# Performance work log

Hardware: AMD Instinct MI355X
Metric: run time of the kernel (lower is better)

## Reference

```python
import jax, jax.numpy as jnp
import numpy as np

B, H, S, D = 2, 16, 8192, 128
NUM_REFLECTIONS = D // 2
ROPE_BASE = 10000.0


def setup_inputs() -> dict:
    key = jax.random.key(0)
    kq, kk, kv = jax.random.split(key, 3)
    q = jax.random.normal(kq, (B, H, S, D), dtype=jnp.float32)
    k = jax.random.normal(kk, (B, H, S, D), dtype=jnp.float32)
    vs = jax.random.normal(kv, (NUM_REFLECTIONS, D), dtype=jnp.float32) * 0.02
    # standard RoPE cos/sin buffer, rotate-half layout: angles duplicated over both halves
    inv_freq = 1.0 / (ROPE_BASE ** (jnp.arange(0, D, 2, dtype=jnp.float32) / D))  # [D/2]
    ang = jnp.arange(S, dtype=jnp.float32)[:, None] * inv_freq[None, :]           # [S, D/2]
    emb = jnp.concatenate([ang, ang], axis=-1)                                    # [S, D]
    cos = jnp.broadcast_to(jnp.cos(emb)[None], (B, S, D))
    sin = jnp.broadcast_to(jnp.sin(emb)[None], (B, S, D))
    return {"q": q, "k": k, "vs": vs, "cos": cos, "sin": sin}


def _householder_matrix(vs):
    # Q = prod of Householder reflections applied left-to-right, as in get_matrix()
    eye = jnp.eye(vs.shape[-1], dtype=vs.dtype)
    def step(Q, v):
        v_norm_sq = jnp.sum(v * v) + 1e-8
        Q = Q - (2.0 / v_norm_sq) * jnp.outer(v, v @ Q)
        return Q, None
    Q, _ = jax.lax.scan(step, eye, vs)
    return Q


def _rotate_half(x):
    d2 = x.shape[-1] // 2
    return jnp.concatenate([-x[..., d2:], x[..., :d2]], axis=-1)


def reference(q, k, vs, cos, sin):
    Q = _householder_matrix(vs)                 # [D, D]
    # inverse transform: x @ Q.T
    qi = jnp.einsum("bhsd,ed->bhse", q, Q)
    ki = jnp.einsum("bhsd,ed->bhse", k, Q)
    c = cos[:, None, :, :]                      # [B,1,S,D] broadcast over heads
    s = sin[:, None, :, :]
    q_rot = qi * c + _rotate_half(qi) * s
    k_rot = ki * c + _rotate_half(ki) * s
    # forward transform: x @ Q
    q_final = jnp.einsum("bhsd,de->bhse", q_rot, Q)
    k_final = jnp.einsum("bhsd,de->bhse", k_rot, Q)
    return (q_final, k_final)
```

## Files before the change

kernel.cpp:

```cpp
#include <hip/hip_runtime.h>

typedef __bf16 bf16x8 __attribute__((ext_vector_type(8)));
typedef __bf16 bf16x4 __attribute__((ext_vector_type(4)));
typedef float  f32x4  __attribute__((ext_vector_type(4)));

static constexpr int kS = 8192;
static constexpr int kD = 128;
static constexpr int kRowsPerTensor = 2 * 16 * kS;
static constexpr int kFragElems = 128 * 128;

__global__ __launch_bounds__(1024) void rnrope_build_q(
    const float* __restrict__ vs,
    __bf16* __restrict__ wsQT,
    __bf16* __restrict__ wsQ) {
  __shared__ float vsh[64 * 128];
  const int tid = threadIdx.x;
  for (int i = tid; i < 2048; i += 1024)
    ((float4*)vsh)[i] = ((const float4*)vs)[i];
  __syncthreads();

  const int col  = blockIdx.x * 16 + (tid >> 6);
  const int lane = tid & 63;

  float qlo = (col == lane)      ? 1.0f : 0.0f;
  float qhi = (col == lane + 64) ? 1.0f : 0.0f;

  for (int r = 0; r < 64; ++r) {
    float vlo = vsh[r * 128 + lane];
    float vhi = vsh[r * 128 + lane + 64];
    float t0 = vlo * qlo + vhi * qhi;
    float t1 = vlo * vlo + vhi * vhi;
    #pragma unroll
    for (int off = 32; off > 0; off >>= 1) {
      t0 += __shfl_xor(t0, off);
      t1 += __shfl_xor(t1, off);
    }
    float cf = 2.0f / (t1 + 1e-8f);
    float sf = cf * t0;
    qlo -= sf * vlo;
    qhi -= sf * vhi;
  }

  {
    const int ks = col >> 5, qd = (col >> 3) & 3, jj = col & 7;
    #pragma unroll
    for (int h = 0; h < 2; ++h) {
      int i = lane + h * 64;
      float val = h ? qhi : qlo;
      int nt = i >> 4;
      int lp = qd * 16 + (i & 15);
      wsQT[((ks * 8 + nt) * 64 + lp) * 8 + jj] = (__bf16)val;
    }
  }
  {
    const int nt = col >> 4;
    const int nn = col & 15;
    #pragma unroll
    for (int h = 0; h < 2; ++h) {
      int i = lane + h * 64;
      float val = h ? qhi : qlo;
      int ks = i >> 5, qd = (i >> 3) & 3, jj = i & 7;
      wsQ[((ks * 8 + nt) * 64 + qd * 16 + nn) * 8 + jj] = (__bf16)val;
    }
  }
}

__global__ __launch_bounds__(512, 4) void rnrope_main(
    const float* __restrict__ qg, const float* __restrict__ kg,
    const __bf16* __restrict__ wsQT, const __bf16* __restrict__ wsQ,
    float* __restrict__ outg) {
  __shared__ __align__(16) __bf16 lds[2 * kFragElems];
  __bf16* ldsB = lds;
  __bf16* ldsA = lds + kFragElems;
  float*  ldsF = (float*)lds;

  const int tid    = threadIdx.x;
  const int blk    = blockIdx.x;
  const int tensor = blk >> 11;
  const int tile   = blk & 2047;
  const float* __restrict__ Xg = tensor ? kg : qg;
  float* __restrict__ Og = outg + (size_t)tensor * (size_t)kRowsPerTensor * kD;
  const int row0 = tile * 128;

  #pragma unroll
  for (int i = 0; i < 4; ++i)
    ((uint4*)ldsB)[tid + i * 512] = ((const uint4*)wsQT)[tid + i * 512];

  #pragma unroll
  for (int it = 0; it < 8; ++it) {
    int f    = tid + it * 512;
    int mloc = f >> 5;
    int q4   = f & 31;
    int k0   = q4 * 4;
    float4 x4 = ((const float4*)(Xg + (size_t)(row0 + mloc) * kD))[q4];
    int ks = k0 >> 5, qd = (k0 >> 3) & 3, j = k0 & 7;
    int w = mloc >> 4, m = mloc & 15;
    int idx = ((w * 4 + ks) * 64 + qd * 16 + m) * 8 + j;
    bf16x4 v;
    v[0] = (__bf16)x4.x; v[1] = (__bf16)x4.y; v[2] = (__bf16)x4.z; v[3] = (__bf16)x4.w;
    *(bf16x4*)(&ldsA[idx]) = v;
  }
  __syncthreads();

  const int w    = tid >> 6;
  const int lane = tid & 63;
  const int qd   = lane >> 4;
  const int cc   = lane & 15;

  f32x4 acc[8];
  #pragma unroll
  for (int nt = 0; nt < 8; ++nt) acc[nt] = (f32x4){0.f, 0.f, 0.f, 0.f};

  #pragma unroll
  for (int ks = 0; ks < 4; ++ks) {
    bf16x8 a = *(const bf16x8*)(&ldsA[((w * 4 + ks) * 64 + lane) * 8]);
    #pragma unroll
    for (int nt = 0; nt < 8; ++nt) {
      bf16x8 b = *(const bf16x8*)(&ldsB[((ks * 8 + nt) * 64 + lane) * 8]);
      acc[nt] = __builtin_amdgcn_mfma_f32_16x16x32_bf16(a, b, acc[nt], 0, 0, 0);
    }
  }

  const int rowb  = row0 + w * 16;
  const int sbase = rowb & (kS - 1);
  const float kNegL = -0.20762050593046967f;
  float invf[4];
  #pragma unroll
  for (int nt = 0; nt < 4; ++nt)
    invf[nt] = exp2f(kNegL * (float)(nt * 16 + cc));
  #pragma unroll
  for (int reg = 0; reg < 4; ++reg) {
    float spos = (float)(sbase + qd * 4 + reg);
    #pragma unroll
    for (int nt = 0; nt < 4; ++nt) {
      float ang = spos * invf[nt];
      float sv, cv;
      __sincosf(ang, &sv, &cv);
      float ylo = acc[nt][reg];
      float yhi = acc[nt + 4][reg];
      acc[nt][reg]     = ylo * cv - yhi * sv;
      acc[nt + 4][reg] = yhi * cv + ylo * sv;
    }
  }

  __syncthreads();

  #pragma unroll
  for (int i = 0; i < 4; ++i)
    ((uint4*)ldsB)[tid + i * 512] = ((const uint4*)wsQ)[tid + i * 512];

  #pragma unroll
  for (int reg = 0; reg < 4; ++reg) {
    int m = qd * 4 + reg;
    #pragma unroll
    for (int nt = 0; nt < 8; ++nt) {
      int e = nt * 16 + cc;
      int ks2 = e >> 5, qd2 = (e >> 3) & 3, j2 = e & 7;
      ldsA[((w * 4 + ks2) * 64 + qd2 * 16 + m) * 8 + j2] = (__bf16)acc[nt][reg];
    }
  }
  __syncthreads();

  #pragma unroll
  for (int nt = 0; nt < 8; ++nt) acc[nt] = (f32x4){0.f, 0.f, 0.f, 0.f};
  #pragma unroll
  for (int ks = 0; ks < 4; ++ks) {
    bf16x8 a = *(const bf16x8*)(&ldsA[((w * 4 + ks) * 64 + lane) * 8]);
    #pragma unroll
    for (int nt = 0; nt < 8; ++nt) {
      bf16x8 b = *(const bf16x8*)(&ldsB[((ks * 8 + nt) * 64 + lane) * 8]);
      acc[nt] = __builtin_amdgcn_mfma_f32_16x16x32_bf16(a, b, acc[nt], 0, 0, 0);
    }
  }

  __syncthreads();
  #pragma unroll
  for (int reg = 0; reg < 4; ++reg) {
    int m = w * 16 + qd * 4 + reg;
    #pragma unroll
    for (int nt = 0; nt < 8; ++nt)
      ldsF[m * kD + nt * 16 + cc] = acc[nt][reg];
  }
  __syncthreads();
  float4* __restrict__ Ot = (float4*)(Og + (size_t)row0 * kD);
  #pragma unroll
  for (int it = 0; it < 8; ++it) {
    int idx = tid + it * 512;
    Ot[idx] = ((const float4*)ldsF)[idx];
  }
}

extern "C" void kernel_launch(void* const* d_in, const int* in_sizes, int n_in,
                              void* d_out, int out_size, void* d_ws, size_t ws_size,
                              hipStream_t stream) {
  const float* q    = (const float*)d_in[0];
  const float* k    = (const float*)d_in[1];
  const float* vs   = (const float*)d_in[2];
  __bf16* wsQT = (__bf16*)d_ws;
  __bf16* wsQ  = wsQT + kFragElems;

  rnrope_build_q<<<8, 1024, 0, stream>>>(vs, wsQT, wsQ);
  rnrope_main<<<4096, 512, 0, stream>>>(q, k, wsQT, wsQ, (float*)d_out);
}
```

Before: 482.7 us.

## Drop LDS staging; compute transposed first GEMM in registers with bpermute re-layout

The main kernel no longer stages the input, the Q matrices or the output through shared memory. Each wave loads its 32 rows straight from global memory into MFMA B-fragments and computes the first product transposed, using a row-major Q read directly from global memory and cache. It then re-lays out the rotated result into A-fragments with ds_bpermute before the second GEMM. Blocks shrink to 256 threads and the barriers go away. In exchange, output stores are scalar and strided rather than coalesced float4 writes, Q fragments are re-read from global or L2 per wave, and register pressure rises.

```diff
diff --git a/kernel.cpp b/kernel.cpp
--- a/kernel.cpp
+++ b/kernel.cpp
@@ -1,18 +1,19 @@
 #include <hip/hip_runtime.h>
 
 typedef __bf16 bf16x8 __attribute__((ext_vector_type(8)));
-typedef __bf16 bf16x4 __attribute__((ext_vector_type(4)));
+typedef __bf16 bf16x2 __attribute__((ext_vector_type(2)));
 typedef float  f32x4  __attribute__((ext_vector_type(4)));
+typedef int    i32x4  __attribute__((ext_vector_type(4)));
 
 static constexpr int kS = 8192;
 static constexpr int kD = 128;
 static constexpr int kRowsPerTensor = 2 * 16 * kS;
-static constexpr int kFragElems = 128 * 128;
+static constexpr int kFragElems = kD * kD;
 
 __global__ __launch_bounds__(1024) void rnrope_build_q(
     const float* __restrict__ vs,
-    __bf16* __restrict__ wsQT,
-    __bf16* __restrict__ wsQ) {
+    __bf16* __restrict__ wsQrm,
+    __bf16* __restrict__ wsQf) {
   __shared__ float vsh[64 * 128];
   const int tid = threadIdx.x;
   for (int i = tid; i < 2048; i += 1024)
@@ -35,23 +36,14 @@
       t0 += __shfl_xor(t0, off);
       t1 += __shfl_xor(t1, off);
     }
-    float cf = 2.0f / (t1 + 1e-8f);
-    float sf = cf * t0;
+    float sf = 2.0f / (t1 + 1e-8f) * t0;
     qlo -= sf * vlo;
     qhi -= sf * vhi;
   }
 
-  {
-    const int ks = col >> 5, qd = (col >> 3) & 3, jj = col & 7;
-    #pragma unroll
-    for (int h = 0; h < 2; ++h) {
-      int i = lane + h * 64;
-      float val = h ? qhi : qlo;
-      int nt = i >> 4;
-      int lp = qd * 16 + (i & 15);
-      wsQT[((ks * 8 + nt) * 64 + lp) * 8 + jj] = (__bf16)val;
-    }
-  }
+  wsQrm[lane * 128 + col]        = (__bf16)qlo;
+  wsQrm[(lane + 64) * 128 + col] = (__bf16)qhi;
+
   {
     const int nt = col >> 4;
     const int nn = col & 15;
@@ -60,145 +52,139 @@
       int i = lane + h * 64;
       float val = h ? qhi : qlo;
       int ks = i >> 5, qd = (i >> 3) & 3, jj = i & 7;
-      wsQ[((ks * 8 + nt) * 64 + qd * 16 + nn) * 8 + jj] = (__bf16)val;
+      wsQf[((ks * 8 + nt) * 64 + qd * 16 + nn) * 8 + jj] = (__bf16)val;
     }
   }
 }
 
-__global__ __launch_bounds__(512, 4) void rnrope_main(
+__global__ __launch_bounds__(256, 3) void rnrope_main(
     const float* __restrict__ qg, const float* __restrict__ kg,
-    const __bf16* __restrict__ wsQT, const __bf16* __restrict__ wsQ,
+    const __bf16* __restrict__ wsQrm, const __bf16* __restrict__ wsQf,
     float* __restrict__ outg) {
-  __shared__ __align__(16) __bf16 lds[2 * kFragElems];
-  __bf16* ldsB = lds;
-  __bf16* ldsA = lds + kFragElems;
-  float*  ldsF = (float*)lds;
+  const int tid  = threadIdx.x;
+  const int wv   = tid >> 6;
+  const int lane = tid & 63;
+  const int qd   = lane >> 4;
+  const int cc   = lane & 15;
 
-  const int tid    = threadIdx.x;
   const int blk    = blockIdx.x;
   const int tensor = blk >> 11;
   const int tile   = blk & 2047;
   const float* __restrict__ Xg = tensor ? kg : qg;
   float* __restrict__ Og = outg + (size_t)tensor * (size_t)kRowsPerTensor * kD;
-  const int row0 = tile * 128;
+  const int r0 = tile * 128 + wv * 32;
 
+  bf16x8 xb[2][4];
   #pragma unroll
-  for (int i = 0; i < 4; ++i)
-    ((uint4*)ldsB)[tid + i * 512] = ((const uint4*)wsQT)[tid + i * 512];
-
-  #pragma unroll
-  for (int it = 0; it < 8; ++it) {
-    int f    = tid + it * 512;
-    int mloc = f >> 5;
-    int q4   = f & 31;
-    int k0   = q4 * 4;
-    float4 x4 = ((const float4*)(Xg + (size_t)(row0 + mloc) * kD))[q4];
-    int ks = k0 >> 5, qd = (k0 >> 3) & 3, j = k0 & 7;
-    int w = mloc >> 4, m = mloc & 15;
-    int idx = ((w * 4 + ks) * 64 + qd * 16 + m) * 8 + j;
-    bf16x4 v;
-    v[0] = (__bf16)x4.x; v[1] = (__bf16)x4.y; v[2] = (__bf16)x4.z; v[3] = (__bf16)x4.w;
-    *(bf16x4*)(&ldsA[idx]) = v;
-  }
-  __syncthreads();
-
-  const int w    = tid >> 6;
-  const int lane = tid & 63;
-  const int qd   = lane >> 4;
-  const int cc   = lane & 15;
-
-  f32x4 acc[8];
-  #pragma unroll
-  for (int nt = 0; nt < 8; ++nt) acc[nt] = (f32x4){0.f, 0.f, 0.f, 0.f};
-
-  #pragma unroll
-  for (int ks = 0; ks < 4; ++ks) {
-    bf16x8 a = *(const bf16x8*)(&ldsA[((w * 4 + ks) * 64 + lane) * 8]);
+  for (int s = 0; s < 2; ++s) {
+    const float* rp = Xg + (size_t)(r0 + s * 16 + cc) * kD + qd * 8;
     #pragma unroll
-    for (int nt = 0; nt < 8; ++nt) {
-      bf16x8 b = *(const bf16x8*)(&ldsB[((ks * 8 + nt) * 64 + lane) * 8]);
-      acc[nt] = __builtin_amdgcn_mfma_f32_16x16x32_bf16(a, b, acc[nt], 0, 0, 0);
+    for (int ks = 0; ks < 4; ++ks) {
+      float4 lo = *(const float4*)(rp + ks * 32);
+      float4 hi = *(const float4*)(rp + ks * 32 + 4);
+      bf16x8 v;
+      v[0] = (__bf16)lo.x; v[1] = (__bf16)lo.y; v[2] = (__bf16)lo.z; v[3] = (__bf16)lo.w;
+      v[4] = (__bf16)hi.x; v[5] = (__bf16)hi.y; v[6] = (__bf16)hi.z; v[7] = (__bf16)hi.w;
+      xb[s][ks] = v;
     }
   }
 
-  const int rowb  = row0 + w * 16;
-  const int sbase = rowb & (kS - 1);
-  const float kNegL = -0.20762050593046967f;
-  float invf[4];
+  f32x4 acc[2][8];
   #pragma unroll
-  for (int nt = 0; nt < 4; ++nt)
-    invf[nt] = exp2f(kNegL * (float)(nt * 16 + cc));
+  for (int s = 0; s < 2; ++s)
+    #pragma unroll
+    for (int mt = 0; mt < 8; ++mt) acc[s][mt] = (f32x4){0.f, 0.f, 0.f, 0.f};
+
   #pragma unroll
-  for (int reg = 0; reg < 4; ++reg) {
-    float spos = (float)(sbase + qd * 4 + reg);
+  for (int mt = 0; mt < 8; ++mt) {
     #pragma unroll
-    for (int nt = 0; nt < 4; ++nt) {
-      float ang = spos * invf[nt];
-      float sv, cv;
-      __sincosf(ang, &sv, &cv);
-      float ylo = acc[nt][reg];
-      float yhi = acc[nt + 4][reg];
-      acc[nt][reg]     = ylo * cv - yhi * sv;
-      acc[nt + 4][reg] = yhi * cv + ylo * sv;
+    for (int ks = 0; ks < 4; ++ks) {
+      bf16x8 a1 = *(const bf16x8*)(wsQrm + (mt * 16 + cc) * kD + ks * 32 + qd * 8);
+      acc[0][mt] = __builtin_amdgcn_mfma_f32_16x16x32_bf16(a1, xb[0][ks], acc[0][mt], 0, 0, 0);
+      acc[1][mt] = __builtin_amdgcn_mfma_f32_16x16x32_bf16(a1, xb[1][ks], acc[1][mt], 0, 0, 0);
     }
   }
 
-  __syncthreads();
-
+  const float kNegL = -0.20762050593046967f;
+  bf16x8 a2[2][4];
   #pragma unroll
-  for (int i = 0; i < 4; ++i)
-    ((uint4*)ldsB)[tid + i * 512] = ((const uint4*)wsQ)[tid + i * 512];
-
-  #pragma unroll
-  for (int reg = 0; reg < 4; ++reg) {
-    int m = qd * 4 + reg;
+  for (int s = 0; s < 2; ++s) {
+    float spos = (float)((r0 + s * 16 + cc) & (kS - 1));
     #pragma unroll
-    for (int nt = 0; nt < 8; ++nt) {
-      int e = nt * 16 + cc;
-      int ks2 = e >> 5, qd2 = (e >> 3) & 3, j2 = e & 7;
-      ldsA[((w * 4 + ks2) * 64 + qd2 * 16 + m) * 8 + j2] = (__bf16)acc[nt][reg];
+    for (int mt = 0; mt < 4; ++mt) {
+      #pragma unroll
+      for (int reg = 0; reg < 4; ++reg) {
+        float fe  = (float)(mt * 16 + qd * 4 + reg);
+        float ang = spos * exp2f(kNegL * fe);
+        float sv, cv;
+        __sincosf(ang, &sv, &cv);
+        float ylo = acc[s][mt][reg];
+        float yhi = acc[s][mt + 4][reg];
+        acc[s][mt][reg]     = ylo * cv - yhi * sv;
+        acc[s][mt + 4][reg] = yhi * cv + ylo * sv;
+      }
     }
-  }
-  __syncthreads();
-
-  #pragma unroll
-  for (int nt = 0; nt < 8; ++nt) acc[nt] = (f32x4){0.f, 0.f, 0.f, 0.f};
-  #pragma unroll
-  for (int ks = 0; ks < 4; ++ks) {
-    bf16x8 a = *(const bf16x8*)(&ldsA[((w * 4 + ks) * 64 + lane) * 8]);
+    int pw[16];
     #pragma unroll
-    for (int nt = 0; nt < 8; ++nt) {
-      bf16x8 b = *(const bf16x8*)(&ldsB[((ks * 8 + nt) * 64 + lane) * 8]);
-      acc[nt] = __builtin_amdgcn_mfma_f32_16x16x32_bf16(a, b, acc[nt], 0, 0, 0);
+    for (int mt = 0; mt < 8; ++mt) {
+      #pragma unroll
+      for (int p = 0; p < 2; ++p) {
+        bf16x2 t;
+        t[0] = (__bf16)acc[s][mt][2 * p];
+        t[1] = (__bf16)acc[s][mt][2 * p + 1];
+        pw[mt * 2 + p] = __builtin_bit_cast(int, t);
+      }
+    }
+    #pragma unroll
+    for (int ks = 0; ks < 4; ++ks) {
+      i32x4 aw;
+      #pragma unroll
+      for (int jw = 0; jw < 4; ++jw) {
+        int srcl = ((((2 * qd + (jw >> 1)) & 3) * 16) + cc) * 4;
+        int wlo = __builtin_amdgcn_ds_bpermute(srcl, pw[4 * ks + (jw & 1)]);
+        int whi = __builtin_amdgcn_ds_bpermute(srcl, pw[4 * ks + 2 + (jw & 1)]);
+        aw[jw] = (qd < 2) ? wlo : whi;
+      }
+      a2[s][ks] = __builtin_bit_cast(bf16x8, aw);
     }
   }
 
-  __syncthreads();
   #pragma unroll
-  for (int reg = 0; reg < 4; ++reg) {
-    int m = w * 16 + qd * 4 + reg;
+  for (int s = 0; s < 2; ++s)
     #pragma unroll
-    for (int nt = 0; nt < 8; ++nt)
-      ldsF[m * kD + nt * 16 + cc] = acc[nt][reg];
+    for (int nt = 0; nt < 8; ++nt) acc[s][nt] = (f32x4){0.f, 0.f, 0.f, 0.f};
+
+  #pragma unroll
+  for (int nt = 0; nt < 8; ++nt) {
+    #pragma unroll
+    for (int ks = 0; ks < 4; ++ks) {
+      bf16x8 b2 = *(const bf16x8*)(wsQf + ((ks * 8 + nt) * 64 + lane) * 8);
+      acc[0][nt] = __builtin_amdgcn_mfma_f32_16x16x32_bf16(a2[0][ks], b2, acc[0][nt], 0, 0, 0);
+      acc[1][nt] = __builtin_amdgcn_mfma_f32_16x16x32_bf16(a2[1][ks], b2, acc[1][nt], 0, 0, 0);
+    }
   }
-  __syncthreads();
-  float4* __restrict__ Ot = (float4*)(Og + (size_t)row0 * kD);
+
   #pragma unroll
-  for (int it = 0; it < 8; ++it) {
-    int idx = tid + it * 512;
-    Ot[idx] = ((const float4*)ldsF)[idx];
+  for (int s = 0; s < 2; ++s) {
+    float* __restrict__ Ob = Og + (size_t)(r0 + s * 16) * kD;
+    #pragma unroll
+    for (int nt = 0; nt < 8; ++nt) {
+      #pragma unroll
+      for (int reg = 0; reg < 4; ++reg)
+        Ob[(qd * 4 + reg) * kD + nt * 16 + cc] = acc[s][nt][reg];
+    }
   }
 }
 
 extern "C" void kernel_launch(void* const* d_in, const int* in_sizes, int n_in,
                               void* d_out, int out_size, void* d_ws, size_t ws_size,
                               hipStream_t stream) {
-  const float* q    = (const float*)d_in[0];
-  const float* k    = (const float*)d_in[1];
-  const float* vs   = (const float*)d_in[2];
-  __bf16* wsQT = (__bf16*)d_ws;
-  __bf16* wsQ  = wsQT + kFragElems;
+  const float* q  = (const float*)d_in[0];
+  const float* k  = (const float*)d_in[1];
+  const float* vs = (const float*)d_in[2];
+  __bf16* wsQrm = (__bf16*)d_ws;
+  __bf16* wsQf  = wsQrm + kFragElems;
 
-  rnrope_build_q<<<8, 1024, 0, stream>>>(vs, wsQT, wsQ);
-  rnrope_main<<<4096, 512, 0, stream>>>(q, k, wsQT, wsQ, (float*)d_out);
+  rnrope_build_q<<<8, 1024, 0, stream>>>(vs, wsQrm, wsQf);
+  rnrope_main<<<4096, 256, 0, stream>>>(q, k, wsQrm, wsQf, (float*)d_out);
 }
```

Measured after the change: 522.1 us. 1.08x slower.
